# Kernel optimization log

Hardware: AMD Instinct MI355X
Metric: run time of the kernel (lower is better)

Reference implementation:

```python
import jax, jax.numpy as jnp
import numpy as np

NODES_PER_GRAPH = 400

def _gcn_conv(x, W, b, src, dst, dis, n):
    # GCNConv with add_self_loops + symmetric degree normalization.
    h = x @ W                                   # [N, C]
    norm = dis[src] * dis[dst]                  # [E]
    agg = jax.ops.segment_sum(h[src] * norm[:, None], dst, num_segments=n)
    agg = agg + (dis * dis)[:, None] * h        # self-loop contribution
    return agg + b


def setup_inputs() -> dict:
    key = jax.random.key(0)
    ks = jax.random.split(key, 8)
    N, E, F, H, C = 51200, 819200, 400, 256, 2
    x = jax.random.normal(ks[0], (N, F), dtype=jnp.float32)
    edge_index = jax.random.randint(ks[1], (2, E), 0, N, dtype=jnp.int32)
    s = 1.0 / np.sqrt(F)
    W1 = jax.random.normal(ks[2], (F, H), dtype=jnp.float32) * s
    b1 = jnp.zeros((H,), dtype=jnp.float32)
    W2 = jax.random.normal(ks[3], (H, H), dtype=jnp.float32) * (1.0 / np.sqrt(H))
    b2 = jnp.zeros((H,), dtype=jnp.float32)
    W3 = jax.random.normal(ks[4], (H, C), dtype=jnp.float32) * (1.0 / np.sqrt(H))
    b3 = jnp.zeros((C,), dtype=jnp.float32)
    return {"x": x, "edge_index": edge_index, "W1": W1, "b1": b1,
            "W2": W2, "b2": b2, "W3": W3, "b3": b3}


def reference(x, edge_index, W1, b1, W2, b2, W3, b3):
    n = x.shape[0]
    src, dst = edge_index[0], edge_index[1]
    # degree after adding self-loops (edge weights = 1), computed on dst
    deg = 1.0 + jax.ops.segment_sum(jnp.ones_like(dst, dtype=x.dtype), dst, num_segments=n)
    dis = jax.lax.rsqrt(deg)
    h = _gcn_conv(x, W1, b1, src, dst, dis, n)
    h = jax.nn.relu(h)  # dropout is identity in eval mode
    h = _gcn_conv(h, W2, b2, src, dst, dis, n)
    h = jax.nn.relu(h)
    h = _gcn_conv(h, W3, b3, src, dst, dis, n)
    # custom mean pool over fixed 400 nodes per graph
    b = n // NODES_PER_GRAPH
    return h.reshape(b, NODES_PER_GRAPH, -1).mean(axis=1)
```

## Files before the change

### kernel.cpp

```cpp
#include <hip/hip_runtime.h>
#include <hip/hip_bf16.h>
#include <stdint.h>

typedef __attribute__((ext_vector_type(8))) __bf16 bf16x8;
typedef __attribute__((ext_vector_type(4))) float f32x4;
typedef __attribute__((ext_vector_type(4))) int i32x4;
typedef unsigned short u16;

#define N_NODES 51200
#define N_EDGES 819200
#define F_IN 400
#define K1Q 448
#define H_DIM 256
#define C_OUT 2
#define N_GRAPHS 128
#define NODES_PER_GRAPH 400
#define NB_SCAN (N_NODES / 256)

__device__ __forceinline__ u16 f2bf(float f) {
  uint32_t u = __builtin_bit_cast(uint32_t, f);
  u = (u + 0x7fffu + ((u >> 16) & 1u)) >> 16;
  return (u16)u;
}
__device__ __forceinline__ float bf2f(u16 s) {
  uint32_t u = ((uint32_t)s) << 16;
  return __builtin_bit_cast(float, u);
}

typedef const __attribute__((address_space(1))) unsigned int* gas_ptr;
typedef __attribute__((address_space(3))) unsigned int* las_ptr;
__device__ __forceinline__ void gl_lds16(const void* g, void* l) {
  __builtin_amdgcn_global_load_lds((gas_ptr)g, (las_ptr)l, 16, 0, 0);
}
__device__ __forceinline__ void wait_vm0()   { asm volatile("s_waitcnt vmcnt(0)" ::: "memory"); }
__device__ __forceinline__ void wait_vm5()   { asm volatile("s_waitcnt vmcnt(5)" ::: "memory"); }
__device__ __forceinline__ void wait_lgkm0() { asm volatile("s_waitcnt lgkmcnt(0)" ::: "memory"); }

__global__ void k_zero(int* __restrict__ p) {
  p[blockIdx.x * 256 + threadIdx.x] = 0;
}

__global__ void k_histrank(const int* __restrict__ dst, int* __restrict__ counts,
                           int* __restrict__ rank, int E) {
  int e = blockIdx.x * 256 + threadIdx.x;
  if (e < E) rank[e] = atomicAdd(&counts[dst[e]], 1);
}

__global__ __launch_bounds__(256) void k_reduce(const int* __restrict__ counts,
                                                int* __restrict__ bsum) {
  int i = blockIdx.x * 256 + threadIdx.x;
  int v = counts[i];
#pragma unroll
  for (int o = 32; o; o >>= 1) v += __shfl_xor(v, o);
  __shared__ int wsum[4];
  if ((threadIdx.x & 63) == 0) wsum[threadIdx.x >> 6] = v;
  __syncthreads();
  if (threadIdx.x == 0) bsum[blockIdx.x] = wsum[0] + wsum[1] + wsum[2] + wsum[3];
}

__global__ __launch_bounds__(256) void k_scantop(const int* __restrict__ bsum,
                                                 int* __restrict__ boff,
                                                 int* __restrict__ off_last) {
  __shared__ int s[256];
  int t = threadIdx.x;
  int v = (t < NB_SCAN) ? bsum[t] : 0;
  s[t] = v;
  __syncthreads();
  for (int d = 1; d < 256; d <<= 1) {
    int u = (t >= d) ? s[t - d] : 0;
    __syncthreads();
    s[t] += u;
    __syncthreads();
  }
  if (t < NB_SCAN) boff[t] = s[t] - v;
  if (t == 0) *off_last = N_EDGES;
}

__global__ __launch_bounds__(256) void k_scanlocal(const int* __restrict__ counts,
                                                   const int* __restrict__ boff,
                                                   int* __restrict__ off,
                                                   float* __restrict__ dis) {
  __shared__ int s[256];
  int t = threadIdx.x;
  int i = blockIdx.x * 256 + t;
  int v = counts[i];
  s[t] = v;
  __syncthreads();
  for (int d = 1; d < 256; d <<= 1) {
    int u = (t >= d) ? s[t - d] : 0;
    __syncthreads();
    s[t] += u;
    __syncthreads();
  }
  int ex = boff[blockIdx.x] + s[t] - v;
  off[i] = ex;
  dis[i] = rsqrtf(1.0f + (float)v);
}

__global__ void k_place(const int* __restrict__ src, const int* __restrict__ dst,
                        const int* __restrict__ rank, const int* __restrict__ off,
                        int* __restrict__ csr_src, int E) {
  int e = blockIdx.x * 256 + threadIdx.x;
  if (e < E) {
    int d = dst[e];
    csr_src[off[d] + rank[e]] = src[e];
  }
}

__global__ __launch_bounds__(256) void k_quantx(const float* __restrict__ x,
                                                int8_t* __restrict__ xq,
                                                float* __restrict__ sx) {
  int wid = threadIdx.x >> 6, lane = threadIdx.x & 63;
  int d = blockIdx.x * 4 + wid;
  float4 v0 = {0.f, 0.f, 0.f, 0.f}, v1 = {0.f, 0.f, 0.f, 0.f};
  if (lane < 50) {
    const float* p = x + (size_t)d * F_IN + lane * 8;
    v0 = *reinterpret_cast<const float4*>(p);
    v1 = *reinterpret_cast<const float4*>(p + 4);
  }
  float m = fmaxf(fmaxf(fmaxf(fabsf(v0.x), fabsf(v0.y)), fmaxf(fabsf(v0.z), fabsf(v0.w))),
                  fmaxf(fmaxf(fabsf(v1.x), fabsf(v1.y)), fmaxf(fabsf(v1.z), fabsf(v1.w))));
#pragma unroll
  for (int o = 32; o; o >>= 1) m = fmaxf(m, __shfl_xor(m, o));
  float inv = (m > 0.f) ? 127.0f / m : 0.f;
  if (lane < 56) {
    uint32_t lo = 0, hi = 0;
    if (lane < 50) {
      int q0 = (int)rintf(v0.x * inv), q1 = (int)rintf(v0.y * inv);
      int q2 = (int)rintf(v0.z * inv), q3 = (int)rintf(v0.w * inv);
      int q4 = (int)rintf(v1.x * inv), q5 = (int)rintf(v1.y * inv);
      int q6 = (int)rintf(v1.z * inv), q7 = (int)rintf(v1.w * inv);
      lo = (uint32_t)(q0 & 255) | ((uint32_t)(q1 & 255) << 8) |
           ((uint32_t)(q2 & 255) << 16) | ((uint32_t)(q3 & 255) << 24);
      hi = (uint32_t)(q4 & 255) | ((uint32_t)(q5 & 255) << 8) |
           ((uint32_t)(q6 & 255) << 16) | ((uint32_t)(q7 & 255) << 24);
    }
    uint2 o8; o8.x = lo; o8.y = hi;
    *reinterpret_cast<uint2*>(xq + (size_t)d * K1Q + lane * 8) = o8;
  }
  if (lane == 0) sx[d] = m * (1.0f / 127.0f);
}

__global__ __launch_bounds__(256) void k_prepw(const float* __restrict__ W1,
                                               const float* __restrict__ W2,
                                               int8_t* __restrict__ w1q,
                                               float* __restrict__ sw,
                                               u16* __restrict__ W2T) {
  int b = blockIdx.x;
  if (b < H_DIM / 4) {
    int wid = threadIdx.x >> 6, lane = threadIdx.x & 63;
    int n = b * 4 + wid;
    float vals[7];
    float m = 0.f;
#pragma unroll
    for (int j = 0; j < 7; ++j) {
      int k = lane + j * 64;
      vals[j] = (k < F_IN) ? W1[(size_t)k * H_DIM + n] : 0.f;
      m = fmaxf(m, fabsf(vals[j]));
    }
#pragma unroll
    for (int o = 32; o; o >>= 1) m = fmaxf(m, __shfl_xor(m, o));
    float inv = (m > 0.f) ? 127.0f / m : 0.f;
#pragma unroll
    for (int j = 0; j < 7; ++j) {
      int k = lane + j * 64;
      w1q[(size_t)n * K1Q + k] = (int8_t)(int)rintf(vals[j] * inv);
    }
    if (lane == 0) sw[n] = m * (1.0f / 127.0f);
  } else {
    int k = b - H_DIM / 4, n = threadIdx.x;
    W2T[n * H_DIM + k] = f2bf(W2[k * H_DIM + n]);
  }
}

__global__ __launch_bounds__(256) void k_mmA8(const int8_t* __restrict__ Aq,
                                              const float* __restrict__ sx,
                                              const int8_t* __restrict__ Bq,
                                              const float* __restrict__ sw,
                                              const float* __restrict__ dis,
                                              int8_t* __restrict__ Cq,
                                              float* __restrict__ rs4) {
  constexpr int KB = K1Q, NS = KB >> 6;
  __shared__ __align__(16) int8_t As[2][64 * 64];
  __shared__ __align__(16) int8_t Bs[2][256 * 64];
  const int tid = threadIdx.x;
  const int lane = tid & 63, wid = tid >> 6;
  const int lr = lane & 15, lg = lane >> 4;
  const int m0 = blockIdx.x * 64;
  const int aRow = tid >> 2;
  const int aSl = ((tid & 3) ^ ((tid >> 3) & 3)) << 4;
  const int bRow16 = lane >> 2;
  const int bSl = ((lane & 3) ^ ((lane >> 3) & 3)) << 4;
  const int rSl = (lg ^ ((lr >> 1) & 3)) << 4;

  auto stage = [&](int s, int b) {
    int k0 = s << 6;
    gl_lds16(Aq + (size_t)(m0 + aRow) * KB + k0 + aSl, (char*)As[b] + wid * 1024);
#pragma unroll
    for (int j = 0; j < 4; ++j) {
      int c = wid * 4 + j;
      gl_lds16(Bq + (size_t)(c * 16 + bRow16) * KB + k0 + bSl, (char*)Bs[b] + c * 1024);
    }
  };

  stage(0, 0);
  stage(1, 1);

  i32x4 acc[4][4] = {};
  for (int k = 0; k < NS; ++k) {
    const int b = k & 1;
    if (k + 1 < NS) wait_vm5(); else wait_vm0();
    __builtin_amdgcn_sched_barrier(0);
    __builtin_amdgcn_s_barrier();
    __builtin_amdgcn_sched_barrier(0);
    i32x4 af[4], bfr[4];
#pragma unroll
    for (int m = 0; m < 4; ++m)
      af[m] = *reinterpret_cast<const i32x4*>(&As[b][(m * 16 + lr) * 64 + rSl]);
#pragma unroll
    for (int n = 0; n < 4; ++n)
      bfr[n] = *reinterpret_cast<const i32x4*>(&Bs[b][(wid * 64 + n * 16 + lr) * 64 + rSl]);
    __builtin_amdgcn_sched_barrier(0);
    wait_lgkm0();
    __builtin_amdgcn_sched_barrier(0);
    __builtin_amdgcn_s_barrier();
    __builtin_amdgcn_sched_barrier(0);
    if (k + 2 < NS) stage(k + 2, b);
    __builtin_amdgcn_sched_barrier(0);
#pragma unroll
    for (int m = 0; m < 4; ++m)
#pragma unroll
      for (int n = 0; n < 4; ++n)
        acc[m][n] = __builtin_amdgcn_mfma_i32_16x16x64_i8(af[m], bfr[n], acc[m][n], 0, 0, 0);
  }

  float swv[4];
#pragma unroll
  for (int n = 0; n < 4; ++n) swv[n] = sw[wid * 64 + n * 16 + lr];
  float pam[4][4];
#pragma unroll
  for (int m = 0; m < 4; ++m)
#pragma unroll
    for (int r = 0; r < 4; ++r) {
      float v0 = fabsf((float)acc[m][0][r] * swv[0]);
      float v1 = fabsf((float)acc[m][1][r] * swv[1]);
      float v2 = fabsf((float)acc[m][2][r] * swv[2]);
      float v3 = fabsf((float)acc[m][3][r] * swv[3]);
      pam[m][r] = fmaxf(fmaxf(v0, v1), fmaxf(v2, v3));
    }
#pragma unroll
  for (int o = 1; o < 16; o <<= 1)
#pragma unroll
    for (int m = 0; m < 4; ++m)
#pragma unroll
      for (int r = 0; r < 4; ++r)
        pam[m][r] = fmaxf(pam[m][r], __shfl_xor(pam[m][r], o));
#pragma unroll
  for (int m = 0; m < 4; ++m)
#pragma unroll
    for (int r = 0; r < 4; ++r) {
      int grow = m0 + m * 16 + lg * 4 + r;
      float fm = fmaxf(pam[m][r], 1e-20f);
      float inv = 127.0f / fm;
      if (lr == 0) rs4[(size_t)grow * 4 + wid] = dis[grow] * sx[grow] * fm * (1.0f / 127.0f);
#pragma unroll
      for (int n = 0; n < 4; ++n) {
        int q = (int)rintf((float)acc[m][n][r] * swv[n] * inv);
        Cq[(size_t)grow * H_DIM + wid * 64 + n * 16 + lr] = (int8_t)q;
      }
    }
}

template <int KB>
__global__ __launch_bounds__(256) void k_mmB(const u16* __restrict__ A,
                                             const u16* __restrict__ BT,
                                             const float* __restrict__ dis,
                                             int8_t* __restrict__ Cq,
                                             float* __restrict__ rs4) {
  constexpr int NS = KB >> 5;
  __shared__ __align__(16) u16 As[2][64 * 32];
  __shared__ __align__(16) u16 Bs[2][256 * 32];
  const int tid = threadIdx.x;
  const int lane = tid & 63, wid = tid >> 6;
  const int lr = lane & 15, lg = lane >> 4;
  const int m0 = blockIdx.x * 64;
  const int sseg = (((lane & 3) ^ ((lane >> 3) & 3)) << 3);
  const int arow = tid >> 2;
  const int brow = lane >> 2;
  const int rs8 = ((lg ^ ((lr >> 1) & 3)) << 3);

  auto stage = [&](int s, int b) {
    int k0 = s << 5;
    gl_lds16(A + (size_t)(m0 + arow) * KB + k0 + sseg, (char*)As[b] + wid * 1024);
#pragma unroll
    for (int j = 0; j < 4; ++j) {
      int c = wid * 4 + j;
      gl_lds16(BT + (size_t)(c * 16 + brow) * KB + k0 + sseg, (char*)Bs[b] + c * 1024);
    }
  };

  stage(0, 0);
  stage(1, 1);

  f32x4 acc[4][4] = {};
  for (int k = 0; k < NS; ++k) {
    const int b = k & 1;
    if (k + 1 < NS) wait_vm5(); else wait_vm0();
    __builtin_amdgcn_sched_barrier(0);
    __builtin_amdgcn_s_barrier();
    __builtin_amdgcn_sched_barrier(0);
    bf16x8 af[4], bfr[4];
#pragma unroll
    for (int m = 0; m < 4; ++m)
      af[m] = *reinterpret_cast<const bf16x8*>(&As[b][(m * 16 + lr) * 32 + rs8]);
#pragma unroll
    for (int n = 0; n < 4; ++n)
      bfr[n] = *reinterpret_cast<const bf16x8*>(&Bs[b][(wid * 64 + n * 16 + lr) * 32 + rs8]);
    __builtin_amdgcn_sched_barrier(0);
    wait_lgkm0();
    __builtin_amdgcn_sched_barrier(0);
    __builtin_amdgcn_s_barrier();
    __builtin_amdgcn_sched_barrier(0);
    if (k + 2 < NS) stage(k + 2, b);
    __builtin_amdgcn_sched_barrier(0);
#pragma unroll
    for (int m = 0; m < 4; ++m)
#pragma unroll
      for (int n = 0; n < 4; ++n)
        acc[m][n] = __builtin_amdgcn_mfma_f32_16x16x32_bf16(af[m], bfr[n], acc[m][n], 0, 0, 0);
  }

  float pam[4][4];
#pragma unroll
  for (int m = 0; m < 4; ++m)
#pragma unroll
    for (int r = 0; r < 4; ++r) {
      float v0 = fabsf(acc[m][0][r]), v1 = fabsf(acc[m][1][r]);
      float v2 = fabsf(acc[m][2][r]), v3 = fabsf(acc[m][3][r]);
      pam[m][r] = fmaxf(fmaxf(v0, v1), fmaxf(v2, v3));
    }
#pragma unroll
  for (int o = 1; o < 16; o <<= 1)
#pragma unroll
    for (int m = 0; m < 4; ++m)
#pragma unroll
      for (int r = 0; r < 4; ++r)
        pam[m][r] = fmaxf(pam[m][r], __shfl_xor(pam[m][r], o));
#pragma unroll
  for (int m = 0; m < 4; ++m)
#pragma unroll
    for (int r = 0; r < 4; ++r) {
      int grow = m0 + m * 16 + lg * 4 + r;
      float fm = fmaxf(pam[m][r], 1e-20f);
      float inv = 127.0f / fm;
      if (lr == 0) rs4[(size_t)grow * 4 + wid] = dis[grow] * fm * (1.0f / 127.0f);
#pragma unroll
      for (int n = 0; n < 4; ++n) {
        int q = (int)rintf(acc[m][n][r] * inv);
        Cq[(size_t)grow * H_DIM + wid * 64 + n * 16 + lr] = (int8_t)q;
      }
    }
}

template <int U>
__device__ __forceinline__ void gath8(const int8_t* __restrict__ tq,
                                      const float* __restrict__ rs4,
                                      const int* __restrict__ csr, int e,
                                      int f0, int qo,
                                      float& a0, float& a1, float& a2, float& a3) {
  int s[U];
  uint32_t v[U];
  float sc[U];
#pragma unroll
  for (int i = 0; i < U; ++i) s[i] = csr[e + i];
#pragma unroll
  for (int i = 0; i < U; ++i) {
    v[i] = *reinterpret_cast<const uint32_t*>(tq + ((size_t)s[i] << 8) + f0);
    sc[i] = rs4[((size_t)s[i] << 2) + qo];
  }
#pragma unroll
  for (int i = 0; i < U; ++i) {
    a0 += sc[i] * (float)(int8_t)(v[i]);
    a1 += sc[i] * (float)(int8_t)(v[i] >> 8);
    a2 += sc[i] * (float)(int8_t)(v[i] >> 16);
    a3 += sc[i] * (float)(int8_t)(v[i] >> 24);
  }
}

template <bool FUSE_T3>
__global__ __launch_bounds__(256) void k_agg(const int8_t* __restrict__ tq,
                                             const float* __restrict__ rs4,
                                             const int* __restrict__ off,
                                             const int* __restrict__ csr,
                                             const float* __restrict__ dis,
                                             const float* __restrict__ bias,
                                             u16* __restrict__ h,
                                             const float* __restrict__ W3,
                                             float* __restrict__ t3, int N) {
  int wid = threadIdx.x >> 6, lane = threadIdx.x & 63;
  int d = blockIdx.x * 4 + wid;
  if (d >= N) return;
  int f0 = lane * 4;
  int qo = lane >> 4;
  float a0, a1, a2, a3;
  {
    uint32_t v = *reinterpret_cast<const uint32_t*>(tq + ((size_t)d << 8) + f0);
    float sc = rs4[((size_t)d << 2) + qo];
    a0 = sc * (float)(int8_t)(v);
    a1 = sc * (float)(int8_t)(v >> 8);
    a2 = sc * (float)(int8_t)(v >> 16);
    a3 = sc * (float)(int8_t)(v >> 24);
  }
  int e = off[d], e1 = off[d + 1];
  while (e + 8 <= e1) { gath8<8>(tq, rs4, csr, e, f0, qo, a0, a1, a2, a3); e += 8; }
  if (e + 4 <= e1) { gath8<4>(tq, rs4, csr, e, f0, qo, a0, a1, a2, a3); e += 4; }
  if (e + 2 <= e1) { gath8<2>(tq, rs4, csr, e, f0, qo, a0, a1, a2, a3); e += 2; }
  if (e < e1)      { gath8<1>(tq, rs4, csr, e, f0, qo, a0, a1, a2, a3); }
  float dd = dis[d];
  float4 bv = *reinterpret_cast<const float4*>(bias + f0);
  float r0 = fmaxf(dd * a0 + bv.x, 0.f);
  float r1 = fmaxf(dd * a1 + bv.y, 0.f);
  float r2 = fmaxf(dd * a2 + bv.z, 0.f);
  float r3 = fmaxf(dd * a3 + bv.w, 0.f);
  if (FUSE_T3) {
    float p0 = r0 * W3[(f0 + 0) * 2]     + r1 * W3[(f0 + 1) * 2]
             + r2 * W3[(f0 + 2) * 2]     + r3 * W3[(f0 + 3) * 2];
    float p1 = r0 * W3[(f0 + 0) * 2 + 1] + r1 * W3[(f0 + 1) * 2 + 1]
             + r2 * W3[(f0 + 2) * 2 + 1] + r3 * W3[(f0 + 3) * 2 + 1];
#pragma unroll
    for (int o = 32; o; o >>= 1) { p0 += __shfl_xor(p0, o); p1 += __shfl_xor(p1, o); }
    if (lane == 0) {
      t3[d * 2] = dd * p0;
      t3[d * 2 + 1] = dd * p1;
    }
  } else {
    ushort4 o;
    o.x = f2bf(r0); o.y = f2bf(r1); o.z = f2bf(r2); o.w = f2bf(r3);
    *reinterpret_cast<ushort4*>(h + ((size_t)d << 8) + f0) = o;
  }
}

__global__ __launch_bounds__(448) void k_aggpool3(const float* __restrict__ t3,
                                                  const int* __restrict__ off,
                                                  const int* __restrict__ csr,
                                                  const float* __restrict__ dis,
                                                  const float* __restrict__ b3,
                                                  float* __restrict__ out) {
  int g = blockIdx.x, t = threadIdx.x;
  int lane = t & 63, wv = t >> 6;
  float a0 = 0.f, a1 = 0.f;
  if (t < NODES_PER_GRAPH) {
    int d = g * NODES_PER_GRAPH + t;
    a0 = t3[d * 2]; a1 = t3[d * 2 + 1];
    int e = off[d], e1 = off[d + 1];
    while (e + 4 <= e1) {
      int s0 = csr[e], s1 = csr[e + 1], s2 = csr[e + 2], s3 = csr[e + 3];
      float2 v0 = *reinterpret_cast<const float2*>(t3 + s0 * 2);
      float2 v1 = *reinterpret_cast<const float2*>(t3 + s1 * 2);
      float2 v2 = *reinterpret_cast<const float2*>(t3 + s2 * 2);
      float2 v3 = *reinterpret_cast<const float2*>(t3 + s3 * 2);
      a0 += v0.x + v1.x + v2.x + v3.x;
      a1 += v0.y + v1.y + v2.y + v3.y;
      e += 4;
    }
    while (e < e1) {
      float2 v = *reinterpret_cast<const float2*>(t3 + csr[e] * 2);
      a0 += v.x; a1 += v.y; ++e;
    }
    float dd = dis[d];
    a0 *= dd; a1 *= dd;
  }
#pragma unroll
  for (int o = 32; o; o >>= 1) { a0 += __shfl_xor(a0, o); a1 += __shfl_xor(a1, o); }
  __shared__ float w0[8], w1[8];
  if (lane == 0) { w0[wv] = a0; w1[wv] = a1; }
  __syncthreads();
  if (t == 0) {
    float s0 = 0.f, s1 = 0.f;
#pragma unroll
    for (int i = 0; i < 7; ++i) { s0 += w0[i]; s1 += w1[i]; }
    out[g * 2]     = s0 * (1.0f / NODES_PER_GRAPH) + b3[0];
    out[g * 2 + 1] = s1 * (1.0f / NODES_PER_GRAPH) + b3[1];
  }
}

extern "C" void kernel_launch(void* const* d_in, const int* in_sizes, int n_in,
                              void* d_out, int out_size, void* d_ws, size_t ws_size,
                              hipStream_t stream) {
  const float* x  = (const float*)d_in[0];
  const int*   ei = (const int*)d_in[1];
  const float* W1 = (const float*)d_in[2];
  const float* b1 = (const float*)d_in[3];
  const float* W2 = (const float*)d_in[4];
  const float* b2 = (const float*)d_in[5];
  const float* W3 = (const float*)d_in[6];
  const float* b3 = (const float*)d_in[7];
  float* out = (float*)d_out;
  const int N = N_NODES, E = N_EDGES;
  const int* src = ei;
  const int* dst = ei + E;

  char* ws = (char*)d_ws;
  size_t o = 0;
  auto alloc = [&](size_t bytes) -> void* {
    void* p = ws + o;
    o += (bytes + 255) & ~(size_t)255;
    return p;
  };
  int8_t* tQ  = (int8_t*)alloc((size_t)N * H_DIM);
  float* rs4  = (float*)alloc((size_t)N * 4 * 4);
  u16* tB     = (u16*)alloc((size_t)N * H_DIM * 2);
  u16* W2T    = (u16*)alloc((size_t)H_DIM * H_DIM * 2);
  float* dis  = (float*)alloc((size_t)N * 4);
  int* counts = (int*)alloc((size_t)N * 4);
  int* rank   = (int*)alloc((size_t)E * 4);
  int* csroff = (int*)alloc((size_t)(N + 1) * 4);
  int* csr    = (int*)alloc((size_t)E * 4);
  float* t3   = (float*)alloc((size_t)N * 2 * 4);
  int* bsum   = (int*)alloc((size_t)NB_SCAN * 4);
  int* boff   = (int*)alloc((size_t)NB_SCAN * 4);
  int8_t* xq  = (int8_t*)alloc((size_t)N * K1Q);
  float* sx   = (float*)alloc((size_t)N * 4);
  int8_t* w1q = (int8_t*)alloc((size_t)H_DIM * K1Q);
  float* sw   = (float*)alloc((size_t)H_DIM * 4);

  k_zero<<<NB_SCAN, 256, 0, stream>>>(counts);
  k_histrank<<<(E + 255) / 256, 256, 0, stream>>>(dst, counts, rank, E);
  k_reduce<<<NB_SCAN, 256, 0, stream>>>(counts, bsum);
  k_scantop<<<1, 256, 0, stream>>>(bsum, boff, csroff + N);
  k_scanlocal<<<NB_SCAN, 256, 0, stream>>>(counts, boff, csroff, dis);
  k_place<<<(E + 255) / 256, 256, 0, stream>>>(src, dst, rank, csroff, csr, E);
  k_quantx<<<N / 4, 256, 0, stream>>>(x, xq, sx);
  k_prepw<<<H_DIM / 4 + H_DIM, 256, 0, stream>>>(W1, W2, w1q, sw, W2T);

  k_mmA8<<<N / 64, 256, 0, stream>>>(xq, sx, w1q, sw, dis, tQ, rs4);
  k_agg<false><<<N / 4, 256, 0, stream>>>(tQ, rs4, csroff, csr, dis, b1, tB, nullptr, nullptr, N);
  k_mmB<H_DIM><<<N / 64, 256, 0, stream>>>(tB, W2T, dis, tQ, rs4);
  k_agg<true><<<N / 4, 256, 0, stream>>>(tQ, rs4, csroff, csr, dis, b2, nullptr, W3, t3, N);
  k_aggpool3<<<N_GRAPHS, 448, 0, stream>>>(t3, csroff, csr, dis, b3, out);
}
```

Baseline: 225.9 us.

## Split aggregation into 64-column feature slices with edge-parallel lane groups

The aggregation kernels now have each block handle one 64-column slice for four nodes. The four 16-lane groups of a wave process different edges in parallel, and a shuffle reduction combines them at the end. Block IDs are remapped so that consecutive blocks cover different slices. The row-scale array is moved to slice-major layout so each slice's scales are contiguous. The fused layer-3 projection now writes per-slice partial sums, and a new small k_sum4 kernel adds them up. The aim is better cache locality for the gathered rows and more memory parallelism per wave, at the cost of four times more blocks, extra shuffles and one additional launch.

Measured after the change: 345.9 us. 53.2% more time.

```diff
diff --git a/kernel.cpp b/kernel.cpp
--- a/kernel.cpp
+++ b/kernel.cpp
@@ -21,10 +21,6 @@
   uint32_t u = __builtin_bit_cast(uint32_t, f);
   u = (u + 0x7fffu + ((u >> 16) & 1u)) >> 16;
   return (u16)u;
-}
-__device__ __forceinline__ float bf2f(u16 s) {
-  uint32_t u = ((uint32_t)s) << 16;
-  return __builtin_bit_cast(float, u);
 }
 
 typedef const __attribute__((address_space(1))) unsigned int* gas_ptr;
@@ -144,7 +140,7 @@
 __global__ __launch_bounds__(256) void k_prepw(const float* __restrict__ W1,
                                                const float* __restrict__ W2,
                                                int8_t* __restrict__ w1q,
-                                               float* __restrict__ sw,
+                                               float* __restrict__ sw1,
                                                u16* __restrict__ W2T) {
   int b = blockIdx.x;
   if (b < H_DIM / 4) {
@@ -166,21 +162,22 @@
       int k = lane + j * 64;
       w1q[(size_t)n * K1Q + k] = (int8_t)(int)rintf(vals[j] * inv);
     }
-    if (lane == 0) sw[n] = m * (1.0f / 127.0f);
+    if (lane == 0) sw1[n] = m * (1.0f / 127.0f);
   } else {
     int k = b - H_DIM / 4, n = threadIdx.x;
     W2T[n * H_DIM + k] = f2bf(W2[k * H_DIM + n]);
   }
 }
 
-__global__ __launch_bounds__(256) void k_mmA8(const int8_t* __restrict__ Aq,
-                                              const float* __restrict__ sx,
-                                              const int8_t* __restrict__ Bq,
-                                              const float* __restrict__ sw,
-                                              const float* __restrict__ dis,
-                                              int8_t* __restrict__ Cq,
-                                              float* __restrict__ rs4) {
-  constexpr int KB = K1Q, NS = KB >> 6;
+template <int KB>
+__global__ __launch_bounds__(256) void k_mm8(const int8_t* __restrict__ Aq,
+                                             const float* __restrict__ srow,
+                                             const int8_t* __restrict__ Bq,
+                                             const float* __restrict__ scol,
+                                             const float* __restrict__ dis,
+                                             int8_t* __restrict__ Cq,
+                                             float* __restrict__ rs4) {
+  constexpr int NS = KB >> 6;
   __shared__ __align__(16) int8_t As[2][64 * 64];
   __shared__ __align__(16) int8_t Bs[2][256 * 64];
   const int tid = threadIdx.x;
@@ -234,18 +231,18 @@
         acc[m][n] = __builtin_amdgcn_mfma_i32_16x16x64_i8(af[m], bfr[n], acc[m][n], 0, 0, 0);
   }
 
-  float swv[4];
-#pragma unroll
-  for (int n = 0; n < 4; ++n) swv[n] = sw[wid * 64 + n * 16 + lr];
+  float scv[4];
+#pragma unroll
+  for (int n = 0; n < 4; ++n) scv[n] = scol[wid * 64 + n * 16 + lr];
   float pam[4][4];
 #pragma unroll
   for (int m = 0; m < 4; ++m)
 #pragma unroll
     for (int r = 0; r < 4; ++r) {
-      float v0 = fabsf((float)acc[m][0][r] * swv[0]);
-      float v1 = fabsf((float)acc[m][1][r] * swv[1]);
-      float v2 = fabsf((float)acc[m][2][r] * swv[2]);
-      float v3 = fabsf((float)acc[m][3][r] * swv[3]);
+      float v0 = fabsf((float)acc[m][0][r] * scv[0]);
+      float v1 = fabsf((float)acc[m][1][r] * scv[1]);
+      float v2 = fabsf((float)acc[m][2][r] * scv[2]);
+      float v3 = fabsf((float)acc[m][3][r] * scv[3]);
       pam[m][r] = fmaxf(fmaxf(v0, v1), fmaxf(v2, v3));
     }
 #pragma unroll
@@ -262,10 +259,11 @@
       int grow = m0 + m * 16 + lg * 4 + r;
       float fm = fmaxf(pam[m][r], 1e-20f);
       float inv = 127.0f / fm;
-      if (lr == 0) rs4[(size_t)grow * 4 + wid] = dis[grow] * sx[grow] * fm * (1.0f / 127.0f);
+      if (lr == 0)
+        rs4[(size_t)wid * N_NODES + grow] = dis[grow] * srow[grow] * fm * (1.0f / 127.0f);
 #pragma unroll
       for (int n = 0; n < 4; ++n) {
-        int q = (int)rintf((float)acc[m][n][r] * swv[n] * inv);
+        int q = (int)rintf((float)acc[m][n][r] * scv[n] * inv);
         Cq[(size_t)grow * H_DIM + wid * 64 + n * 16 + lr] = (int8_t)q;
       }
     }
@@ -353,7 +351,7 @@
       int grow = m0 + m * 16 + lg * 4 + r;
       float fm = fmaxf(pam[m][r], 1e-20f);
       float inv = 127.0f / fm;
-      if (lr == 0) rs4[(size_t)grow * 4 + wid] = dis[grow] * fm * (1.0f / 127.0f);
+      if (lr == 0) rs4[(size_t)wid * N_NODES + grow] = dis[grow] * fm * (1.0f / 127.0f);
 #pragma unroll
       for (int n = 0; n < 4; ++n) {
         int q = (int)rintf(acc[m][n][r] * inv);
@@ -362,82 +360,102 @@
     }
 }
 
-template <int U>
-__device__ __forceinline__ void gath8(const int8_t* __restrict__ tq,
-                                      const float* __restrict__ rs4,
-                                      const int* __restrict__ csr, int e,
-                                      int f0, int qo,
-                                      float& a0, float& a1, float& a2, float& a3) {
-  int s[U];
-  uint32_t v[U];
-  float sc[U];
-#pragma unroll
-  for (int i = 0; i < U; ++i) s[i] = csr[e + i];
-#pragma unroll
-  for (int i = 0; i < U; ++i) {
-    v[i] = *reinterpret_cast<const uint32_t*>(tq + ((size_t)s[i] << 8) + f0);
-    sc[i] = rs4[((size_t)s[i] << 2) + qo];
-  }
-#pragma unroll
-  for (int i = 0; i < U; ++i) {
-    a0 += sc[i] * (float)(int8_t)(v[i]);
-    a1 += sc[i] * (float)(int8_t)(v[i] >> 8);
-    a2 += sc[i] * (float)(int8_t)(v[i] >> 16);
-    a3 += sc[i] * (float)(int8_t)(v[i] >> 24);
-  }
-}
-
 template <bool FUSE_T3>
-__global__ __launch_bounds__(256) void k_agg(const int8_t* __restrict__ tq,
-                                             const float* __restrict__ rs4,
-                                             const int* __restrict__ off,
-                                             const int* __restrict__ csr,
-                                             const float* __restrict__ dis,
-                                             const float* __restrict__ bias,
-                                             u16* __restrict__ h,
-                                             const float* __restrict__ W3,
-                                             float* __restrict__ t3, int N) {
-  int wid = threadIdx.x >> 6, lane = threadIdx.x & 63;
-  int d = blockIdx.x * 4 + wid;
-  if (d >= N) return;
-  int f0 = lane * 4;
-  int qo = lane >> 4;
-  float a0, a1, a2, a3;
-  {
-    uint32_t v = *reinterpret_cast<const uint32_t*>(tq + ((size_t)d << 8) + f0);
-    float sc = rs4[((size_t)d << 2) + qo];
+__global__ __launch_bounds__(256) void k_aggs(const int8_t* __restrict__ tq,
+                                              const float* __restrict__ rs4,
+                                              const int* __restrict__ off,
+                                              const int* __restrict__ csr,
+                                              const float* __restrict__ dis,
+                                              const float* __restrict__ bias,
+                                              u16* __restrict__ h,
+                                              const float* __restrict__ W3,
+                                              float* __restrict__ t3p) {
+  const int bid = blockIdx.x;
+  const int wid = threadIdx.x >> 6, lane = threadIdx.x & 63;
+  const int sl = (bid & 7) >> 1;
+  const int j = ((bid >> 3) << 1) | (bid & 1);
+  const int d = j * 4 + wid;
+  const int g = lane >> 4;
+  const int c = lane & 15;
+  const int colb = sl * 64 + c * 4;
+  const float* rs4s = rs4 + (size_t)sl * N_NODES;
+
+  float a0 = 0.f, a1 = 0.f, a2 = 0.f, a3 = 0.f;
+  if (g == 0) {
+    uint32_t v = *reinterpret_cast<const uint32_t*>(tq + ((size_t)d << 8) + colb);
+    float sc = rs4s[d];
     a0 = sc * (float)(int8_t)(v);
     a1 = sc * (float)(int8_t)(v >> 8);
     a2 = sc * (float)(int8_t)(v >> 16);
     a3 = sc * (float)(int8_t)(v >> 24);
   }
   int e = off[d], e1 = off[d + 1];
-  while (e + 8 <= e1) { gath8<8>(tq, rs4, csr, e, f0, qo, a0, a1, a2, a3); e += 8; }
-  if (e + 4 <= e1) { gath8<4>(tq, rs4, csr, e, f0, qo, a0, a1, a2, a3); e += 4; }
-  if (e + 2 <= e1) { gath8<2>(tq, rs4, csr, e, f0, qo, a0, a1, a2, a3); e += 2; }
-  if (e < e1)      { gath8<1>(tq, rs4, csr, e, f0, qo, a0, a1, a2, a3); }
+  while (e + 16 <= e1) {
+    int i0 = csr[e + g], i1 = csr[e + 4 + g], i2 = csr[e + 8 + g], i3 = csr[e + 12 + g];
+    uint32_t v0 = *reinterpret_cast<const uint32_t*>(tq + ((size_t)i0 << 8) + colb);
+    uint32_t v1 = *reinterpret_cast<const uint32_t*>(tq + ((size_t)i1 << 8) + colb);
+    uint32_t v2 = *reinterpret_cast<const uint32_t*>(tq + ((size_t)i2 << 8) + colb);
+    uint32_t v3 = *reinterpret_cast<const uint32_t*>(tq + ((size_t)i3 << 8) + colb);
+    float c0 = rs4s[i0], c1 = rs4s[i1], c2 = rs4s[i2], c3 = rs4s[i3];
+    a0 += c0 * (float)(int8_t)(v0) + c1 * (float)(int8_t)(v1)
+        + c2 * (float)(int8_t)(v2) + c3 * (float)(int8_t)(v3);
+    a1 += c0 * (float)(int8_t)(v0 >> 8) + c1 * (float)(int8_t)(v1 >> 8)
+        + c2 * (float)(int8_t)(v2 >> 8) + c3 * (float)(int8_t)(v3 >> 8);
+    a2 += c0 * (float)(int8_t)(v0 >> 16) + c1 * (float)(int8_t)(v1 >> 16)
+        + c2 * (float)(int8_t)(v2 >> 16) + c3 * (float)(int8_t)(v3 >> 16);
+    a3 += c0 * (float)(int8_t)(v0 >> 24) + c1 * (float)(int8_t)(v1 >> 24)
+        + c2 * (float)(int8_t)(v2 >> 24) + c3 * (float)(int8_t)(v3 >> 24);
+    e += 16;
+  }
+  while (e < e1) {
+    bool valid = (e + g) < e1;
+    int idx = valid ? csr[e + g] : 0;
+    float sc = valid ? rs4s[idx] : 0.f;
+    uint32_t v = *reinterpret_cast<const uint32_t*>(tq + ((size_t)idx << 8) + colb);
+    a0 += sc * (float)(int8_t)(v);
+    a1 += sc * (float)(int8_t)(v >> 8);
+    a2 += sc * (float)(int8_t)(v >> 16);
+    a3 += sc * (float)(int8_t)(v >> 24);
+    e += 4;
+  }
+  a0 += __shfl_xor(a0, 16); a0 += __shfl_xor(a0, 32);
+  a1 += __shfl_xor(a1, 16); a1 += __shfl_xor(a1, 32);
+  a2 += __shfl_xor(a2, 16); a2 += __shfl_xor(a2, 32);
+  a3 += __shfl_xor(a3, 16); a3 += __shfl_xor(a3, 32);
+
   float dd = dis[d];
-  float4 bv = *reinterpret_cast<const float4*>(bias + f0);
+  float4 bv = *reinterpret_cast<const float4*>(bias + colb);
   float r0 = fmaxf(dd * a0 + bv.x, 0.f);
   float r1 = fmaxf(dd * a1 + bv.y, 0.f);
   float r2 = fmaxf(dd * a2 + bv.z, 0.f);
   float r3 = fmaxf(dd * a3 + bv.w, 0.f);
   if (FUSE_T3) {
-    float p0 = r0 * W3[(f0 + 0) * 2]     + r1 * W3[(f0 + 1) * 2]
-             + r2 * W3[(f0 + 2) * 2]     + r3 * W3[(f0 + 3) * 2];
-    float p1 = r0 * W3[(f0 + 0) * 2 + 1] + r1 * W3[(f0 + 1) * 2 + 1]
-             + r2 * W3[(f0 + 2) * 2 + 1] + r3 * W3[(f0 + 3) * 2 + 1];
-#pragma unroll
-    for (int o = 32; o; o >>= 1) { p0 += __shfl_xor(p0, o); p1 += __shfl_xor(p1, o); }
+    float p0 = r0 * W3[(colb + 0) * 2]     + r1 * W3[(colb + 1) * 2]
+             + r2 * W3[(colb + 2) * 2]     + r3 * W3[(colb + 3) * 2];
+    float p1 = r0 * W3[(colb + 0) * 2 + 1] + r1 * W3[(colb + 1) * 2 + 1]
+             + r2 * W3[(colb + 2) * 2 + 1] + r3 * W3[(colb + 3) * 2 + 1];
+#pragma unroll
+    for (int o = 1; o < 16; o <<= 1) { p0 += __shfl_xor(p0, o); p1 += __shfl_xor(p1, o); }
     if (lane == 0) {
-      t3[d * 2] = dd * p0;
-      t3[d * 2 + 1] = dd * p1;
+      t3p[(size_t)d * 8 + sl * 2]     = dd * p0;
+      t3p[(size_t)d * 8 + sl * 2 + 1] = dd * p1;
     }
   } else {
-    ushort4 o;
-    o.x = f2bf(r0); o.y = f2bf(r1); o.z = f2bf(r2); o.w = f2bf(r3);
-    *reinterpret_cast<ushort4*>(h + ((size_t)d << 8) + f0) = o;
-  }
+    if (g == 0) {
+      ushort4 o;
+      o.x = f2bf(r0); o.y = f2bf(r1); o.z = f2bf(r2); o.w = f2bf(r3);
+      *reinterpret_cast<ushort4*>(h + ((size_t)d << 8) + colb) = o;
+    }
+  }
+}
+
+__global__ __launch_bounds__(256) void k_sum4(const float* __restrict__ t3p,
+                                              float* __restrict__ t3) {
+  int d = blockIdx.x * 256 + threadIdx.x;
+  f32x4 lo = *reinterpret_cast<const f32x4*>(t3p + (size_t)d * 8);
+  f32x4 hi = *reinterpret_cast<const f32x4*>(t3p + (size_t)d * 8 + 4);
+  t3[d * 2]     = lo[0] + lo[2] + hi[0] + hi[2];
+  t3[d * 2 + 1] = lo[1] + lo[3] + hi[1] + hi[3];
 }
 
 __global__ __launch_bounds__(448) void k_aggpool3(const float* __restrict__ t3,
@@ -496,7 +514,7 @@
   const float* W3 = (const float*)d_in[6];
   const float* b3 = (const float*)d_in[7];
   float* out = (float*)d_out;
-  const int N = N_NODES, E = N_EDGES;
+  const int E = N_EDGES;
   const int* src = ei;
   const int* dst = ei + E;
 
@@ -507,35 +525,39 @@
     o += (bytes + 255) & ~(size_t)255;
     return p;
   };
-  int8_t* tQ  = (int8_t*)alloc((size_t)N * H_DIM);
-  float* rs4  = (float*)alloc((size_t)N * 4 * 4);
-  u16* tB     = (u16*)alloc((size_t)N * H_DIM * 2);
-  u16* W2T    = (u16*)alloc((size_t)H_DIM * H_DIM * 2);
-  float* dis  = (float*)alloc((size_t)N * 4);
-  int* counts = (int*)alloc((size_t)N * 4);
-  int* rank   = (int*)alloc((size_t)E * 4);
-  int* csroff = (int*)alloc((size_t)(N + 1) * 4);
-  int* csr    = (int*)alloc((size_t)E * 4);
-  float* t3   = (float*)alloc((size_t)N * 2 * 4);
-  int* bsum   = (int*)alloc((size_t)NB_SCAN * 4);
-  int* boff   = (int*)alloc((size_t)NB_SCAN * 4);
-  int8_t* xq  = (int8_t*)alloc((size_t)N * K1Q);
-  float* sx   = (float*)alloc((size_t)N * 4);
-  int8_t* w1q = (int8_t*)alloc((size_t)H_DIM * K1Q);
-  float* sw   = (float*)alloc((size_t)H_DIM * 4);
+  int8_t* tQ   = (int8_t*)alloc((size_t)N_NODES * H_DIM);
+  float* rs4   = (float*)alloc((size_t)N_NODES * 4 * 4);
+  u16* tB      = (u16*)alloc((size_t)N_NODES * H_DIM * 2);
+  u16* W2T     = (u16*)alloc((size_t)H_DIM * H_DIM * 2);
+  float* dis   = (float*)alloc((size_t)N_NODES * 4);
+  int* counts  = (int*)alloc((size_t)N_NODES * 4);
+  int* rank    = (int*)alloc((size_t)E * 4);
+  int* csroff  = (int*)alloc((size_t)(N_NODES + 1) * 4);
+  int* csr     = (int*)alloc((size_t)E * 4);
+  float* t3    = (float*)alloc((size_t)N_NODES * 2 * 4);
+  float* t3p   = (float*)alloc((size_t)N_NODES * 8 * 4);
+  int* bsum    = (int*)alloc((size_t)NB_SCAN * 4);
+  int* boff    = (int*)alloc((size_t)NB_SCAN * 4);
+  int8_t* xq   = (int8_t*)alloc((size_t)N_NODES * K1Q);
+  float* sx    = (float*)alloc((size_t)N_NODES * 4);
+  int8_t* w1q  = (int8_t*)alloc((size_t)H_DIM * K1Q);
+  float* sw1   = (float*)alloc((size_t)H_DIM * 4);
 
   k_zero<<<NB_SCAN, 256, 0, stream>>>(counts);
   k_histrank<<<(E + 255) / 256, 256, 0, stream>>>(dst, counts, rank, E);
   k_reduce<<<NB_SCAN, 256, 0, stream>>>(counts, bsum);
-  k_scantop<<<1, 256, 0, stream>>>(bsum, boff, csroff + N);
+  k_scantop<<<1, 256, 0, stream>>>(bsum, boff, csroff + N_NODES);
   k_scanlocal<<<NB_SCAN, 256, 0, stream>>>(counts, boff, csroff, dis);
   k_place<<<(E + 255) / 256, 256, 0, stream>>>(src, dst, rank, csroff, csr, E);
-  k_quantx<<<N / 4, 256, 0, stream>>>(x, xq, sx);
-  k_prepw<<<H_DIM / 4 + H_DIM, 256, 0, stream>>>(W1, W2, w1q, sw, W2T);
-
-  k_mmA8<<<N / 64, 256, 0, stream>>>(xq, sx, w1q, sw, dis, tQ, rs4);
-  k_agg<false><<<N / 4, 256, 0, stream>>>(tQ, rs4, csroff, csr, dis, b1, tB, nullptr, nullptr, N);
-  k_mmB<H_DIM><<<N / 64, 256, 0, stream>>>(tB, W2T, dis, tQ, rs4);
-  k_agg<true><<<N / 4, 256, 0, stream>>>(tQ, rs4, csroff, csr, dis, b2, nullptr, W3, t3, N);
+  k_quantx<<<N_NODES / 4, 256, 0, stream>>>(x, xq, sx);
+  k_prepw<<<H_DIM / 4 + H_DIM, 256, 0, stream>>>(W1, W2, w1q, sw1, W2T);
+
+  k_mm8<K1Q><<<N_NODES / 64, 256, 0, stream>>>(xq, sx, w1q, sw1, dis, tQ, rs4);
+  k_aggs<false><<<N_NODES, 256, 0, stream>>>(tQ, rs4, csroff, csr, dis, b1,
+                                             tB, nullptr, nullptr);
+  k_mmB<H_DIM><<<N_NODES / 64, 256, 0, stream>>>(tB, W2T, dis, tQ, rs4);
+  k_aggs<true><<<N_NODES, 256, 0, stream>>>(tQ, rs4, csroff, csr, dis, b2,
+                                            nullptr, W3, t3p);
+  k_sum4<<<NB_SCAN, 256, 0, stream>>>(t3p, t3);
   k_aggpool3<<<N_GRAPHS, 448, 0, stream>>>(t3, csroff, csr, dis, b3, out);
 }
```
